# Kernel optimization log

Measured on AMD Instinct MI355X. Metric: run time of the kernel, lower is better.

## Reference

```python
import jax, jax.numpy as jnp
import numpy as np

CODEBOOK_SIZE = 1024
EMB_DIM = 256
BETA = 0.25


def setup_inputs() -> dict:
    key = jax.random.key(0)
    k1, k2 = jax.random.split(key)
    z = jax.random.normal(k1, (8, EMB_DIM, 16, 16, 16), dtype=jnp.float32)
    # torch init: uniform(-1/K, 1/K)
    emb = jax.random.uniform(k2, (CODEBOOK_SIZE, EMB_DIM), dtype=jnp.float32,
                             minval=-1.0 / CODEBOOK_SIZE, maxval=1.0 / CODEBOOK_SIZE)
    return {"z": z, "emb": emb}


def reference(z, emb):
    b, c, h, w, dd = z.shape
    K = emb.shape[0]
    # (b c h w d) -> (b h w d, c)
    zf = jnp.transpose(z, (0, 2, 3, 4, 1)).reshape(-1, c)  # [N, C]
    d = ((zf ** 2).sum(axis=1, keepdims=True)
         + (emb ** 2).sum(axis=1)
         - 2.0 * zf @ emb.T)  # [N, K]
    mean_distance = jnp.mean(d)
    idx = jnp.argmin(d, axis=1)  # [N]
    # one-hot @ codebook == gather
    zq = jnp.take(emb, idx, axis=0)  # [N, C]
    zq = jnp.transpose(zq.reshape(b, h, w, dd, c), (0, 4, 1, 2, 3))  # [b,c,h,w,d]
    loss = (jnp.mean((jax.lax.stop_gradient(zq) - z) ** 2)
            + BETA * jnp.mean((zq - jax.lax.stop_gradient(z)) ** 2))
    # straight-through estimator
    zq_st = z + jax.lax.stop_gradient(zq - z)
    # perplexity from code usage histogram (== mean of one-hot encodings)
    counts = jnp.zeros((K,), dtype=z.dtype).at[idx].add(1.0)
    e_mean = counts / idx.shape[0]
    perplexity = jnp.exp(-jnp.sum(e_mean * jnp.log(e_mean + 1e-10)))
    return zq_st, loss, perplexity, idx, mean_distance
```

## Files before the change

### kernel.cpp

```cpp
#include <hip/hip_runtime.h>
#include <math.h>

#define C 256
#define K 1024
#define SS 4096
#define NB 8
#define NN 32768
#define ZQ_ELEMS 8388608
#define OUT_LOSS 8388608
#define OUT_PERP 8388609
#define OUT_IDX  8388610
#define OUT_MD   8421378

#define WS_SZ2   0
#define WS_SE2   1
#define WS_LOSS  2
#define WS_ZSUM  8
#define WS_ESUM  264
#define WS_CNT   520
#define WS_E2R   1544
#define WS_Z2N   2568
#define WS_FLG   35336
#define WS_EH    68608
#define WS_EL    199680
#define WS_CAND  330752

#define TC_FACT 9.6e-7f
#define TF_FACT 6.0e-7f
#define CAP 4
#define CAP_BIG 16
#define OV 7

typedef __attribute__((ext_vector_type(8))) short short8;
typedef __attribute__((ext_vector_type(4))) float f32x4;
typedef unsigned short u16;

__device__ inline u16 f2bf(float x) {
  unsigned u = __float_as_uint(x);
  unsigned r = (u + 0x7fffu + ((u >> 16) & 1u)) >> 16;
  return (u16)r;
}
__device__ inline float bf2f(u16 h) { return __uint_as_float(((unsigned)h) << 16); }

__device__ __forceinline__ void gl_lds16(const u16* g, u16* l) {
  __builtin_amdgcn_global_load_lds(
      (const __attribute__((address_space(1))) unsigned int*)g,
      (__attribute__((address_space(3))) unsigned int*)l,
      16, 0, 0);
}

__device__ inline float np_sumsq_256(const float* __restrict__ a) {
  float tot = 0.f;
  #pragma unroll
  for (int h = 0; h < 2; ++h) {
    const float* p = a + 128 * h;
    float r[8];
    #pragma unroll
    for (int j = 0; j < 8; ++j) r[j] = __fmul_rn(p[j], p[j]);
    for (int i = 8; i < 128; i += 8) {
      #pragma unroll
      for (int j = 0; j < 8; ++j) {
        float v = p[i + j];
        r[j] = __fadd_rn(r[j], __fmul_rn(v, v));
      }
    }
    float s01 = __fadd_rn(r[0], r[1]);
    float s23 = __fadd_rn(r[2], r[3]);
    float s45 = __fadd_rn(r[4], r[5]);
    float s67 = __fadd_rn(r[6], r[7]);
    float res = __fadd_rn(__fadd_rn(s01, s23), __fadd_rn(s45, s67));
    tot = (h == 0) ? res : __fadd_rn(tot, res);
  }
  return tot;
}

__global__ __launch_bounds__(256)
void emb_prep_k(const float* __restrict__ emb, float* __restrict__ ws,
                u16* __restrict__ eh, u16* __restrict__ el) {
  int r0 = blockIdx.x * 16;
  int t = threadIdx.x;
  float s = 0.f;
  #pragma unroll
  for (int i = 0; i < 16; ++i) {
    size_t idx = (size_t)(r0 + i) * C + t;
    float v = emb[idx];
    s += v;
    u16 h = f2bf(v);
    eh[idx] = h;
    el[idx] = f2bf(v - bf2f(h));
  }
  atomicAdd(&ws[WS_ESUM + t], s);
  if (t < 16) {
    float e2 = np_sumsq_256(emb + (size_t)(r0 + t) * C);
    ws[WS_E2R + r0 + t] = e2;
    atomicAdd(&ws[WS_SE2], e2);
  }
}

#define MROWS 64
#define ZS_STRIDE 260

__global__ __launch_bounds__(256)
void prep_z_k(const float* __restrict__ z, float* __restrict__ ws,
              u16* __restrict__ zh_g, u16* __restrict__ zl_g) {
  __shared__ float zs[MROWS * ZS_STRIDE];
  const int t = threadIdx.x;
  const int n0 = blockIdx.x * MROWS;
  const int b = n0 / SS;
  const int s0 = n0 % SS;
  {
    const int sl = t & 63, cg = t >> 6;
    const float* zb = z + (size_t)b * C * SS + s0 + sl;
    #pragma unroll
    for (int i = 0; i < 16; ++i) {
      int c = (cg * 16 + i) * 4;
      float4 v;
      v.x = zb[(size_t)(c + 0) * SS];
      v.y = zb[(size_t)(c + 1) * SS];
      v.z = zb[(size_t)(c + 2) * SS];
      v.w = zb[(size_t)(c + 3) * SS];
      *(float4*)&zs[sl * ZS_STRIDE + c] = v;
    }
  }
  __syncthreads();
  {
    float s = 0.f;
    #pragma unroll 8
    for (int r = 0; r < MROWS; ++r) s += zs[r * ZS_STRIDE + t];
    atomicAdd(&ws[WS_ZSUM + t], s);
  }
  {
    #pragma unroll
    for (int i = 0; i < 8; ++i) {
      int q = i * 256 + t;
      int row = q >> 5;
      int c0 = (q & 31) * 8;
      float4 va = *(const float4*)&zs[row * ZS_STRIDE + c0];
      float4 vb = *(const float4*)&zs[row * ZS_STRIDE + c0 + 4];
      float f[8] = {va.x, va.y, va.z, va.w, vb.x, vb.y, vb.z, vb.w};
      short8 hv, lv;
      #pragma unroll
      for (int j = 0; j < 8; ++j) {
        u16 h = f2bf(f[j]);
        hv[j] = (short)h;
        lv[j] = (short)f2bf(f[j] - bf2f(h));
      }
      size_t off = (size_t)(n0 + row) * C + c0;
      *(short8*)&zh_g[off] = hv;
      *(short8*)&zl_g[off] = lv;
    }
  }
  if (t < MROWS) {
    float z2 = np_sumsq_256(&zs[t * ZS_STRIDE]);
    ws[WS_Z2N + n0 + t] = z2;
    #pragma unroll
    for (int off = 32; off; off >>= 1) z2 += __shfl_down(z2, off);
    if (t == 0) atomicAdd(&ws[WS_SZ2], z2);
  }
}

#define BM 64
#define BN 128
#define CH 64

__global__ __launch_bounds__(256, 2)
void vq_mfma_k(const u16* __restrict__ zh_g, const u16* __restrict__ zl_g,
               const u16* __restrict__ eh_g, const u16* __restrict__ el_g,
               const float* __restrict__ e2row, const float* __restrict__ z2np,
               float* __restrict__ out_idx,
               int* __restrict__ qarr, u16* __restrict__ cand) {
  extern __shared__ u16 smem_u16[];
  u16* Ah = smem_u16;
  u16* Al = Ah + BM * CH;
  u16* Bh = Al + BM * CH;
  u16* Bl = Bh + BN * CH;
  float* e2s = (float*)(Bl + BN * CH);
  float* mv1 = e2s + BN;
  float* mi1 = mv1 + 2 * BM;
  float* z2s = mi1 + 2 * BM;
  float* lval = z2s + BM;
  unsigned* Mlds = (unsigned*)(lval + BM * CAP_BIG);
  unsigned* cntl = Mlds + BM;
  u16* lidx = (u16*)(cntl + BM);

  const int t = threadIdx.x;
  const int lane = t & 63;
  const int wid = t >> 6;
  const int wm = wid >> 1, wn = wid & 1;
  const int quad = lane >> 4, lr = lane & 15;
  const int row0 = blockIdx.x * BM;
  const int wrow = lane >> 3;
  const int pl = wrow * C + ((lane & 7) ^ wrow) * 8;

  if (t < BM) {
    z2s[t] = z2np[row0 + t];
    Mlds[t] = 0x7F800000u;
    cntl[t] = 0u;
  }

  float v1[8], i1f[8];
  #pragma unroll
  for (int s = 0; s < 8; ++s) { v1[s] = 3.4e38f; i1f[s] = 0.f; }

  for (int nt = 0; nt < K / BN; ++nt) {
    const int kc0 = nt * BN;
    __syncthreads();
    if (t < BN) e2s[t] = e2row[kc0 + t];

    f32x4 acc[2][4];
    #pragma unroll
    for (int mi = 0; mi < 2; ++mi)
      #pragma unroll
      for (int ni = 0; ni < 4; ++ni) acc[mi][ni] = (f32x4){0.f, 0.f, 0.f, 0.f};

    for (int ch = 0; ch < C / CH; ++ch) {
      const int c0 = ch * CH;
      __syncthreads();
      #pragma unroll
      for (int i = 0; i < 2; ++i) {
        int grow = (wid * 2 + i) * 8;
        size_t src = (size_t)(row0 + grow) * C + c0 + pl;
        gl_lds16(&zh_g[src], &Ah[grow * CH]);
        gl_lds16(&zl_g[src], &Al[grow * CH]);
      }
      #pragma unroll
      for (int i = 0; i < 4; ++i) {
        int grow = (wid * 4 + i) * 8;
        size_t src = (size_t)(kc0 + grow) * C + c0 + pl;
        gl_lds16(&eh_g[src], &Bh[grow * CH]);
        gl_lds16(&el_g[src], &Bl[grow * CH]);
      }
      __syncthreads();
      #pragma unroll
      for (int s = 0; s < 2; ++s) {
        const int q = s * 4 + quad;
        short8 afh[2], afl[2];
        #pragma unroll
        for (int mi = 0; mi < 2; ++mi) {
          int rowl = wm * 32 + mi * 16 + lr;
          int jp = q ^ (rowl & 7);
          afh[mi] = *(short8*)&Ah[rowl * CH + jp * 8];
          afl[mi] = *(short8*)&Al[rowl * CH + jp * 8];
        }
        #pragma unroll
        for (int ni = 0; ni < 4; ++ni) {
          int rowb = wn * 64 + ni * 16 + lr;
          int jp = q ^ (rowb & 7);
          short8 bh = *(short8*)&Bh[rowb * CH + jp * 8];
          short8 bl = *(short8*)&Bl[rowb * CH + jp * 8];
          #pragma unroll
          for (int mi = 0; mi < 2; ++mi) {
            acc[mi][ni] = __builtin_amdgcn_mfma_f32_16x16x32_bf16(afh[mi], bh, acc[mi][ni], 0, 0, 0);
            acc[mi][ni] = __builtin_amdgcn_mfma_f32_16x16x32_bf16(afh[mi], bl, acc[mi][ni], 0, 0, 0);
            acc[mi][ni] = __builtin_amdgcn_mfma_f32_16x16x32_bf16(afl[mi], bh, acc[mi][ni], 0, 0, 0);
          }
        }
      }
    }
    #pragma unroll
    for (int mi = 0; mi < 2; ++mi)
      #pragma unroll
      for (int r = 0; r < 4; ++r) {
        int row = wm * 32 + mi * 16 + quad * 4 + r;
        float z2r = z2s[row];
        float m4 = 3.4e38f;
        #pragma unroll
        for (int ni = 0; ni < 4; ++ni) {
          int col = wn * 64 + ni * 16 + lr;
          float dq = __fsub_rn(__fadd_rn(z2r, e2s[col]),
                               __fmul_rn(2.f, acc[mi][ni][r]));
          m4 = fminf(m4, dq);
        }
        atomicMin(&Mlds[row], __float_as_uint(m4));
      }
    __syncthreads();
    #pragma unroll
    for (int mi = 0; mi < 2; ++mi)
      #pragma unroll
      for (int r = 0; r < 4; ++r) {
        int row = wm * 32 + mi * 16 + quad * 4 + r;
        float z2r = z2s[row];
        float M = __uint_as_float(Mlds[row]);
        float thr = fmaf(M, TC_FACT, M);
        int slot = mi * 4 + r;
        #pragma unroll
        for (int ni = 0; ni < 4; ++ni) {
          int col = wn * 64 + ni * 16 + lr;
          float dq = __fsub_rn(__fadd_rn(z2r, e2s[col]),
                               __fmul_rn(2.f, acc[mi][ni][r]));
          if (dq < v1[slot]) { v1[slot] = dq; i1f[slot] = (float)(kc0 + col); }
          if (dq < thr) {
            unsigned p = atomicAdd(&cntl[row], 1u);
            if (p < CAP_BIG) {
              lval[row * CAP_BIG + p] = dq;
              lidx[row * CAP_BIG + p] = (u16)(kc0 + col);
            }
          }
        }
      }
  }
  #pragma unroll
  for (int off = 1; off < 16; off <<= 1) {
    #pragma unroll
    for (int s = 0; s < 8; ++s) {
      float ov1 = __shfl_xor(v1[s], off);
      float oi1 = __shfl_xor(i1f[s], off);
      bool take = (ov1 < v1[s]) || (ov1 == v1[s] && oi1 < i1f[s]);
      if (take) { v1[s] = ov1; i1f[s] = oi1; }
    }
  }
  __syncthreads();
  if (lr == 0) {
    #pragma unroll
    for (int mi = 0; mi < 2; ++mi)
      #pragma unroll
      for (int r = 0; r < 4; ++r) {
        int slot = mi * 4 + r;
        int row = wm * 32 + mi * 16 + quad * 4 + r;
        mv1[wn * BM + row] = v1[slot];
        mi1[wn * BM + row] = i1f[slot];
      }
  }
  __syncthreads();
  if (t < BM) {
    float a1 = mv1[t], ai = mi1[t];
    float c1 = mv1[BM + t], ci = mi1[BM + t];
    bool take = (c1 < a1) || (c1 == a1 && ci < ai);
    float b1 = take ? c1 : a1;
    float bi = take ? ci : ai;
    out_idx[row0 + t] = bi;
    unsigned raw = cntl[t];
    float tf = fmaf(b1, TF_FACT, b1);
    int c = 0;
    u16 keep[CAP];
    bool ov = raw > (unsigned)CAP_BIG;
    if (!ov) {
      for (unsigned j = 0; j < raw; ++j) {
        if (lval[t * CAP_BIG + j] <= tf) {
          if (c < CAP) keep[c] = lidx[t * CAP_BIG + j];
          ++c;
        }
      }
      if (c > CAP) ov = true;
    }
    if (ov || c > 1) {
      int q = atomicAdd(&qarr[0], 1);
      int cc = ov ? OV : c;
      qarr[1 + q] = (row0 + t) | (cc << 16);
      if (!ov)
        #pragma unroll
        for (int j = 0; j < CAP; ++j)
          cand[(size_t)q * CAP + j] = (j < c) ? keep[j] : (u16)0;
    }
  }
}

__global__ __launch_bounds__(256)
void fixup_k(const float* __restrict__ z, const float* __restrict__ emb,
             const float* __restrict__ e2np, const float* __restrict__ z2np,
             const int* __restrict__ qarr, const u16* __restrict__ cand,
             float* __restrict__ out_idx) {
  int qcnt = qarr[0];
  if (qcnt > NN) qcnt = NN;
  const int t = threadIdx.x;
  const int lane = t & 63, w = t >> 6;
  for (int q = blockIdx.x * 4 + w; q < qcnt; q += gridDim.x * 4) {
    int e = qarr[1 + q];
    int n = e & 0xffff;
    int c = e >> 16;
    int b = n >> 12, s = n & (SS - 1);
    float z2 = z2np[n];
    const float* zb = z + (((size_t)b * C) << 12) + s;
    float4 zv;
    zv.x = zb[((size_t)(lane * 4 + 0)) << 12];
    zv.y = zb[((size_t)(lane * 4 + 1)) << 12];
    zv.z = zb[((size_t)(lane * 4 + 2)) << 12];
    zv.w = zb[((size_t)(lane * 4 + 3)) << 12];
    float bestd = 3.4e38f;
    int besti = 0x7fffffff;
    const int nc = (c == OV) ? K : c;
    for (int j = 0; j < nc; ++j) {
      int kk = (c == OV) ? j : (int)cand[(size_t)q * CAP + j];
      const float4 ev = *(const float4*)&emb[(size_t)kk * C + lane * 4];
      double acc = (double)zv.x * (double)ev.x;
      acc = fma((double)zv.y, (double)ev.y, acc);
      acc = fma((double)zv.z, (double)ev.z, acc);
      acc = fma((double)zv.w, (double)ev.w, acc);
      #pragma unroll
      for (int off = 32; off; off >>= 1) acc += __shfl_xor(acc, off);
      float g  = (float)acc;
      float t1 = __fadd_rn(z2, e2np[kk]);
      float d  = __fsub_rn(t1, __fmul_rn(2.f, g));
      if (d < bestd || (d == bestd && kk < besti)) { bestd = d; besti = kk; }
    }
    if (lane == 0) out_idx[n] = (float)besti;
  }
}

#define GROWS 64
__global__ __launch_bounds__(256)
void gather2_k(const float* __restrict__ z, const float* __restrict__ emb,
               float* __restrict__ out, float* __restrict__ ws,
               float* __restrict__ counts) {
  __shared__ float eb[GROWS * 257];
  __shared__ int idxs[GROWS];
  __shared__ float sc[4];
  const int t = threadIdx.x;
  const int n0 = blockIdx.x * GROWS;
  const int b = n0 >> 12;
  const int s0 = n0 & (SS - 1);
  if (t < GROWS) {
    int id = (int)out[OUT_IDX + n0 + t];
    idxs[t] = id;
    atomicAdd(&counts[id], 1.0f);
  }
  __syncthreads();
  #pragma unroll
  for (int i = 0; i < 16; ++i) {
    int q = i * 256 + t;
    int row = q >> 6, c4 = q & 63;
    float4 v = *(const float4*)&emb[(size_t)idxs[row] * C + c4 * 4];
    int base = row * 257 + c4 * 4;
    eb[base + 0] = v.x; eb[base + 1] = v.y;
    eb[base + 2] = v.z; eb[base + 3] = v.w;
  }
  __syncthreads();
  const int sl = t & 63, cg = t >> 6;
  const float* zb = z + (size_t)b * C * SS + s0 + sl;
  float* ob = out + (size_t)b * C * SS + s0 + sl;
  float l = 0.f;
  #pragma unroll 4
  for (int i = 0; i < 64; ++i) {
    int c = cg * 64 + i;
    float q = eb[sl * 257 + c];
    float zv = zb[(size_t)c * SS];
    float d = q - zv;
    l += d * d;
    ob[(size_t)c * SS] = q;
  }
  #pragma unroll
  for (int off = 32; off; off >>= 1) l += __shfl_down(l, off);
  int lane = t & 63, w = t >> 6;
  if (lane == 0) sc[w] = l;
  __syncthreads();
  if (t == 0)
    atomicAdd(&ws[WS_LOSS], sc[0] + sc[1] + sc[2] + sc[3]);
}

__global__ void finalize_k(const float* __restrict__ ws, float* __restrict__ out) {
  __shared__ float sc[8];
  int t = threadIdx.x;
  float ent = 0.f;
  #pragma unroll
  for (int k = t; k < K; k += 256) {
    float em = ws[WS_CNT + k] * (1.0f / NN);
    ent += em * logf(em + 1e-10f);
  }
  float zd = ws[WS_ZSUM + t] * ws[WS_ESUM + t];
  #pragma unroll
  for (int off = 32; off; off >>= 1) {
    ent += __shfl_down(ent, off);
    zd  += __shfl_down(zd, off);
  }
  int lane = t & 63, w = t >> 6;
  if (lane == 0) { sc[w] = ent; sc[4 + w] = zd; }
  __syncthreads();
  if (t == 0) {
    ent = sc[0] + sc[1] + sc[2] + sc[3];
    zd  = sc[4] + sc[5] + sc[6] + sc[7];
    out[OUT_LOSS] = 1.25f * ws[WS_LOSS] * (1.0f / ZQ_ELEMS);
    out[OUT_PERP] = expf(-ent);
    out[OUT_MD]   = ws[WS_SZ2] * (1.0f / NN) + ws[WS_SE2] * (1.0f / K)
                  - 2.0f * zd * (1.0f / ((float)NN * (float)K));
  }
}

extern "C" void kernel_launch(void* const* d_in, const int* in_sizes, int n_in,
                              void* d_out, int out_size, void* d_ws, size_t ws_size,
                              hipStream_t stream) {
  const float* z   = (const float*)d_in[0];
  const float* emb = (const float*)d_in[1];
  float* out = (float*)d_out;
  float* ws  = (float*)d_ws;
  int* qarr = (int*)(ws + WS_FLG);
  u16* cand = (u16*)(ws + WS_CAND);
  u16* eh_g = (u16*)(ws + WS_EH);
  u16* el_g = (u16*)(ws + WS_EL);
  u16* zh_g = (u16*)d_out;
  u16* zl_g = zh_g + (size_t)ZQ_ELEMS;
  (void)in_sizes; (void)n_in; (void)out_size; (void)ws_size;

  hipMemsetAsync(d_ws, 0, WS_E2R * sizeof(float), stream);
  hipMemsetAsync(ws + WS_FLG, 0, sizeof(int), stream);
  emb_prep_k<<<64, 256, 0, stream>>>(emb, ws, eh_g, el_g);
  prep_z_k<<<NN / MROWS, 256, 0, stream>>>(z, ws, zh_g, zl_g);
  size_t lds = (size_t)(2 * BM * CH + 2 * BN * CH) * sizeof(u16)
             + (size_t)(BN + 4 * BM + BM + BM * CAP_BIG) * sizeof(float)
             + (size_t)(2 * BM) * sizeof(unsigned)
             + (size_t)(BM * CAP_BIG) * sizeof(u16);
  vq_mfma_k<<<NN / BM, 256, lds, stream>>>(zh_g, zl_g, eh_g, el_g,
                                           ws + WS_E2R, ws + WS_Z2N,
                                           out + OUT_IDX, qarr, cand);
  fixup_k<<<2048, 256, 0, stream>>>(z, emb, ws + WS_E2R, ws + WS_Z2N,
                                    qarr, cand, out + OUT_IDX);
  gather2_k<<<NN / GROWS, 256, 0, stream>>>(z, emb, out, ws, ws + WS_CNT);
  finalize_k<<<1, 256, 0, stream>>>(ws, out);
}
```

Baseline: 225.2 us.

## Drop bf16 split-precision to single bf16 MFMA with double-buffered loads

Replaces the three-term bf16 hi/lo split GEMM with a single bf16 MFMA pass, which removes the low-part buffers and cuts MFMA work and memory traffic to about a third. Candidate thresholds are widened so the fixup kernel can still recover exact argmins despite the coarser distances. The main loop is flattened into one pipelined loop with double-buffered LDS loads. The per-tile min is now computed by shuffles before candidates are collected, replacing the second pass. The risk is more candidates overflowing the caps and more fixup work.

```diff
diff --git a/kernel.cpp b/kernel.cpp
--- a/kernel.cpp
+++ b/kernel.cpp
@@ -22,11 +22,10 @@
 #define WS_Z2N   2568
 #define WS_FLG   35336
 #define WS_EH    68608
-#define WS_EL    199680
 #define WS_CAND  330752
 
-#define TC_FACT 9.6e-7f
-#define TF_FACT 6.0e-7f
+#define TC_FACT 3.2e-6f
+#define TF_FACT 2.4e-6f
 #define CAP 4
 #define CAP_BIG 16
 #define OV 7
@@ -76,7 +75,7 @@
 
 __global__ __launch_bounds__(256)
 void emb_prep_k(const float* __restrict__ emb, float* __restrict__ ws,
-                u16* __restrict__ eh, u16* __restrict__ el) {
+                u16* __restrict__ eh) {
   int r0 = blockIdx.x * 16;
   int t = threadIdx.x;
   float s = 0.f;
@@ -85,9 +84,7 @@
     size_t idx = (size_t)(r0 + i) * C + t;
     float v = emb[idx];
     s += v;
-    u16 h = f2bf(v);
-    eh[idx] = h;
-    el[idx] = f2bf(v - bf2f(h));
+    eh[idx] = f2bf(v);
   }
   atomicAdd(&ws[WS_ESUM + t], s);
   if (t < 16) {
@@ -102,7 +99,7 @@
 
 __global__ __launch_bounds__(256)
 void prep_z_k(const float* __restrict__ z, float* __restrict__ ws,
-              u16* __restrict__ zh_g, u16* __restrict__ zl_g) {
+              u16* __restrict__ zh_g) {
   __shared__ float zs[MROWS * ZS_STRIDE];
   const int t = threadIdx.x;
   const int n0 = blockIdx.x * MROWS;
@@ -138,16 +135,10 @@
       float4 va = *(const float4*)&zs[row * ZS_STRIDE + c0];
       float4 vb = *(const float4*)&zs[row * ZS_STRIDE + c0 + 4];
       float f[8] = {va.x, va.y, va.z, va.w, vb.x, vb.y, vb.z, vb.w};
-      short8 hv, lv;
-      #pragma unroll
-      for (int j = 0; j < 8; ++j) {
-        u16 h = f2bf(f[j]);
-        hv[j] = (short)h;
-        lv[j] = (short)f2bf(f[j] - bf2f(h));
-      }
-      size_t off = (size_t)(n0 + row) * C + c0;
-      *(short8*)&zh_g[off] = hv;
-      *(short8*)&zl_g[off] = lv;
+      short8 hv;
+      #pragma unroll
+      for (int j = 0; j < 8; ++j) hv[j] = (short)f2bf(f[j]);
+      *(short8*)&zh_g[(size_t)(n0 + row) * C + c0] = hv;
     }
   }
   if (t < MROWS) {
@@ -164,20 +155,15 @@
 #define CH 64
 
 __global__ __launch_bounds__(256, 2)
-void vq_mfma_k(const u16* __restrict__ zh_g, const u16* __restrict__ zl_g,
-               const u16* __restrict__ eh_g, const u16* __restrict__ el_g,
+void vq_mfma_k(const u16* __restrict__ zh_g, const u16* __restrict__ eh_g,
                const float* __restrict__ e2row, const float* __restrict__ z2np,
                float* __restrict__ out_idx,
                int* __restrict__ qarr, u16* __restrict__ cand) {
   extern __shared__ u16 smem_u16[];
-  u16* Ah = smem_u16;
-  u16* Al = Ah + BM * CH;
-  u16* Bh = Al + BM * CH;
-  u16* Bl = Bh + BN * CH;
-  float* e2s = (float*)(Bl + BN * CH);
-  float* mv1 = e2s + BN;
-  float* mi1 = mv1 + 2 * BM;
-  float* z2s = mi1 + 2 * BM;
+  u16* Ah2 = smem_u16;
+  u16* Bh2 = Ah2 + 2 * BM * CH;
+  float* e2s = (float*)(Bh2 + 2 * BN * CH);
+  float* z2s = e2s + BN;
   float* lval = z2s + BM;
   unsigned* Mlds = (unsigned*)(lval + BM * CAP_BIG);
   unsigned* cntl = Mlds + BM;
@@ -198,107 +184,116 @@
     cntl[t] = 0u;
   }
 
+  {
+    #pragma unroll
+    for (int i = 0; i < 2; ++i) {
+      int grow = (wid * 2 + i) * 8;
+      gl_lds16(&zh_g[(size_t)(row0 + grow) * C + pl], &Ah2[grow * CH]);
+    }
+    #pragma unroll
+    for (int i = 0; i < 4; ++i) {
+      int grow = (wid * 4 + i) * 8;
+      gl_lds16(&eh_g[(size_t)grow * C + pl], &Bh2[grow * CH]);
+    }
+  }
+  __syncthreads();
+
   float v1[8], i1f[8];
   #pragma unroll
   for (int s = 0; s < 8; ++s) { v1[s] = 3.4e38f; i1f[s] = 0.f; }
 
-  for (int nt = 0; nt < K / BN; ++nt) {
-    const int kc0 = nt * BN;
-    __syncthreads();
-    if (t < BN) e2s[t] = e2row[kc0 + t];
-
-    f32x4 acc[2][4];
-    #pragma unroll
-    for (int mi = 0; mi < 2; ++mi)
-      #pragma unroll
-      for (int ni = 0; ni < 4; ++ni) acc[mi][ni] = (f32x4){0.f, 0.f, 0.f, 0.f};
-
-    for (int ch = 0; ch < C / CH; ++ch) {
-      const int c0 = ch * CH;
-      __syncthreads();
+  f32x4 acc[2][4];
+  #pragma unroll
+  for (int mi = 0; mi < 2; ++mi)
+    #pragma unroll
+    for (int ni = 0; ni < 4; ++ni) acc[mi][ni] = (f32x4){0.f, 0.f, 0.f, 0.f};
+
+  int p = 0;
+  for (int it = 0; it < 32; ++it) {
+    const int nt = it >> 2, ch = it & 3;
+    if (ch == 0 && t < BN) e2s[t] = e2row[nt * BN + t];
+    if (it < 31) {
+      const int ntn = (it + 1) >> 2, chn = (it + 1) & 3;
+      const int c0n = chn * CH;
+      u16* Ab = Ah2 + (p ^ 1) * (BM * CH);
+      u16* Bb = Bh2 + (p ^ 1) * (BN * CH);
       #pragma unroll
       for (int i = 0; i < 2; ++i) {
         int grow = (wid * 2 + i) * 8;
-        size_t src = (size_t)(row0 + grow) * C + c0 + pl;
-        gl_lds16(&zh_g[src], &Ah[grow * CH]);
-        gl_lds16(&zl_g[src], &Al[grow * CH]);
+        gl_lds16(&zh_g[(size_t)(row0 + grow) * C + c0n + pl], &Ab[grow * CH]);
       }
       #pragma unroll
       for (int i = 0; i < 4; ++i) {
         int grow = (wid * 4 + i) * 8;
-        size_t src = (size_t)(kc0 + grow) * C + c0 + pl;
-        gl_lds16(&eh_g[src], &Bh[grow * CH]);
-        gl_lds16(&el_g[src], &Bl[grow * CH]);
+        gl_lds16(&eh_g[(size_t)(ntn * BN + grow) * C + c0n + pl], &Bb[grow * CH]);
       }
-      __syncthreads();
+    }
+    {
+      const u16* Ab = Ah2 + p * (BM * CH);
+      const u16* Bb = Bh2 + p * (BN * CH);
       #pragma unroll
       for (int s = 0; s < 2; ++s) {
         const int q = s * 4 + quad;
-        short8 afh[2], afl[2];
+        short8 af[2];
         #pragma unroll
         for (int mi = 0; mi < 2; ++mi) {
           int rowl = wm * 32 + mi * 16 + lr;
           int jp = q ^ (rowl & 7);
-          afh[mi] = *(short8*)&Ah[rowl * CH + jp * 8];
-          afl[mi] = *(short8*)&Al[rowl * CH + jp * 8];
+          af[mi] = *(const short8*)&Ab[rowl * CH + jp * 8];
         }
         #pragma unroll
         for (int ni = 0; ni < 4; ++ni) {
           int rowb = wn * 64 + ni * 16 + lr;
           int jp = q ^ (rowb & 7);
-          short8 bh = *(short8*)&Bh[rowb * CH + jp * 8];
-          short8 bl = *(short8*)&Bl[rowb * CH + jp * 8];
+          short8 bh = *(const short8*)&Bb[rowb * CH + jp * 8];
           #pragma unroll
-          for (int mi = 0; mi < 2; ++mi) {
-            acc[mi][ni] = __builtin_amdgcn_mfma_f32_16x16x32_bf16(afh[mi], bh, acc[mi][ni], 0, 0, 0);
-            acc[mi][ni] = __builtin_amdgcn_mfma_f32_16x16x32_bf16(afh[mi], bl, acc[mi][ni], 0, 0, 0);
-            acc[mi][ni] = __builtin_amdgcn_mfma_f32_16x16x32_bf16(afl[mi], bh, acc[mi][ni], 0, 0, 0);
-          }
+          for (int mi = 0; mi < 2; ++mi)
+            acc[mi][ni] = __builtin_amdgcn_mfma_f32_16x16x32_bf16(af[mi], bh, acc[mi][ni], 0, 0, 0);
         }
       }
     }
-    #pragma unroll
-    for (int mi = 0; mi < 2; ++mi)
-      #pragma unroll
-      for (int r = 0; r < 4; ++r) {
-        int row = wm * 32 + mi * 16 + quad * 4 + r;
-        float z2r = z2s[row];
-        float m4 = 3.4e38f;
+    if (ch == 3) {
+      const int kc0 = nt * BN;
+      #pragma unroll
+      for (int mi = 0; mi < 2; ++mi)
         #pragma unroll
-        for (int ni = 0; ni < 4; ++ni) {
-          int col = wn * 64 + ni * 16 + lr;
-          float dq = __fsub_rn(__fadd_rn(z2r, e2s[col]),
-                               __fmul_rn(2.f, acc[mi][ni][r]));
-          m4 = fminf(m4, dq);
+        for (int r = 0; r < 4; ++r) {
+          const int slot = mi * 4 + r;
+          const int row = wm * 32 + mi * 16 + quad * 4 + r;
+          const float z2r = z2s[row];
+          float dqv[4];
+          #pragma unroll
+          for (int ni = 0; ni < 4; ++ni)
+            dqv[ni] = __fsub_rn(__fadd_rn(z2r, e2s[wn * 64 + ni * 16 + lr]),
+                                __fmul_rn(2.f, acc[mi][ni][r]));
+          float mm = fminf(fminf(dqv[0], dqv[1]), fminf(dqv[2], dqv[3]));
+          #pragma unroll
+          for (int off = 1; off < 16; off <<= 1)
+            mm = fminf(mm, __shfl_xor(mm, off));
+          float Mst = __uint_as_float(Mlds[row]);
+          float base = fminf(mm, Mst);
+          float thr = fmaf(base, TC_FACT, base);
+          #pragma unroll
+          for (int ni = 0; ni < 4; ++ni) {
+            float dq = dqv[ni];
+            int col = kc0 + wn * 64 + ni * 16 + lr;
+            if (dq < v1[slot]) { v1[slot] = dq; i1f[slot] = (float)col; }
+            if (dq < thr) {
+              unsigned pp = atomicAdd(&cntl[row], 1u);
+              if (pp < CAP_BIG) {
+                lval[row * CAP_BIG + pp] = dq;
+                lidx[row * CAP_BIG + pp] = (u16)col;
+              }
+            }
+            acc[mi][ni][r] = 0.f;
+          }
+          if (lr == 0) atomicMin(&Mlds[row], __float_as_uint(mm));
         }
-        atomicMin(&Mlds[row], __float_as_uint(m4));
-      }
+    }
     __syncthreads();
-    #pragma unroll
-    for (int mi = 0; mi < 2; ++mi)
-      #pragma unroll
-      for (int r = 0; r < 4; ++r) {
-        int row = wm * 32 + mi * 16 + quad * 4 + r;
-        float z2r = z2s[row];
-        float M = __uint_as_float(Mlds[row]);
-        float thr = fmaf(M, TC_FACT, M);
-        int slot = mi * 4 + r;
-        #pragma unroll
-        for (int ni = 0; ni < 4; ++ni) {
-          int col = wn * 64 + ni * 16 + lr;
-          float dq = __fsub_rn(__fadd_rn(z2r, e2s[col]),
-                               __fmul_rn(2.f, acc[mi][ni][r]));
-          if (dq < v1[slot]) { v1[slot] = dq; i1f[slot] = (float)(kc0 + col); }
-          if (dq < thr) {
-            unsigned p = atomicAdd(&cntl[row], 1u);
-            if (p < CAP_BIG) {
-              lval[row * CAP_BIG + p] = dq;
-              lidx[row * CAP_BIG + p] = (u16)(kc0 + col);
-            }
-          }
-        }
-      }
-  }
+    p ^= 1;
+  }
+
   #pragma unroll
   for (int off = 1; off < 16; off <<= 1) {
     #pragma unroll
@@ -310,6 +305,8 @@
     }
   }
   __syncthreads();
+  float* mv1 = (float*)Ah2;
+  float* mi1 = mv1 + 2 * BM;
   if (lr == 0) {
     #pragma unroll
     for (int mi = 0; mi < 2; ++mi)
@@ -485,20 +482,18 @@
   int* qarr = (int*)(ws + WS_FLG);
   u16* cand = (u16*)(ws + WS_CAND);
   u16* eh_g = (u16*)(ws + WS_EH);
-  u16* el_g = (u16*)(ws + WS_EL);
   u16* zh_g = (u16*)d_out;
-  u16* zl_g = zh_g + (size_t)ZQ_ELEMS;
   (void)in_sizes; (void)n_in; (void)out_size; (void)ws_size;
 
   hipMemsetAsync(d_ws, 0, WS_E2R * sizeof(float), stream);
   hipMemsetAsync(ws + WS_FLG, 0, sizeof(int), stream);
-  emb_prep_k<<<64, 256, 0, stream>>>(emb, ws, eh_g, el_g);
-  prep_z_k<<<NN / MROWS, 256, 0, stream>>>(z, ws, zh_g, zl_g);
+  emb_prep_k<<<64, 256, 0, stream>>>(emb, ws, eh_g);
+  prep_z_k<<<NN / MROWS, 256, 0, stream>>>(z, ws, zh_g);
   size_t lds = (size_t)(2 * BM * CH + 2 * BN * CH) * sizeof(u16)
-             + (size_t)(BN + 4 * BM + BM + BM * CAP_BIG) * sizeof(float)
+             + (size_t)(BN + BM + BM * CAP_BIG) * sizeof(float)
              + (size_t)(2 * BM) * sizeof(unsigned)
              + (size_t)(BM * CAP_BIG) * sizeof(u16);
-  vq_mfma_k<<<NN / BM, 256, lds, stream>>>(zh_g, zl_g, eh_g, el_g,
+  vq_mfma_k<<<NN / BM, 256, lds, stream>>>(zh_g, eh_g,
                                            ws + WS_E2R, ws + WS_Z2N,
                                            out + OUT_IDX, qarr, cand);
   fixup_k<<<2048, 256, 0, stream>>>(z, emb, ws + WS_E2R, ws + WS_Z2N,
```

Result: slower. 661.2 us (+193.6%).
